# Optimization experiments

Measured on AMD Instinct MI355X. Metric: run time of the kernel, lower is better.

The kernel has to match this reference:

```python
import jax, jax.numpy as jnp
import numpy as np
from jax import lax

K = 3      # kernel size
PAD = 1    # padding (stride=1, dilation=1, single offset group)


def _deform_conv2d(x, off, weight, bias):
    # x: [B,C,H,W], off: [B,2*K*K,H,W] (y,x per tap), weight: [O,C,K,K], bias: [O]
    B, C, H, W = x.shape
    KK = K * K
    off = off.reshape(B, KK, 2, H, W)
    off_y, off_x = off[:, :, 0], off[:, :, 1]          # [B,KK,H,W]

    kh = jnp.repeat(jnp.arange(K, dtype=x.dtype), K)   # [KK] tap row offsets
    kw = jnp.tile(jnp.arange(K, dtype=x.dtype), K)     # [KK] tap col offsets
    py = (jnp.arange(H, dtype=x.dtype)[None, None, :, None] - PAD
          + kh[None, :, None, None] + off_y)           # [B,KK,H,W] sample rows
    px = (jnp.arange(W, dtype=x.dtype)[None, None, None, :] - PAD
          + kw[None, :, None, None] + off_x)           # [B,KK,H,W] sample cols

    y0 = jnp.floor(py); x0 = jnp.floor(px)
    wy1 = py - y0; wx1 = px - x0
    wy0 = 1.0 - wy1; wx0 = 1.0 - wx1

    bidx = jnp.arange(B)[:, None, None, None]

    def gather(iy, ix):
        # zero outside the input (torchvision semantics)
        valid = (iy >= 0) & (iy < H) & (ix >= 0) & (ix < W)
        iyc = jnp.clip(iy, 0, H - 1).astype(jnp.int32)
        ixc = jnp.clip(ix, 0, W - 1).astype(jnp.int32)
        v = x[bidx, :, iyc, ixc]                       # [B,KK,H,W,C]
        return v * valid[..., None].astype(x.dtype)

    samp = (gather(y0, x0)           * (wy0 * wx0)[..., None]
            + gather(y0, x0 + 1)     * (wy0 * wx1)[..., None]
            + gather(y0 + 1, x0)     * (wy1 * wx0)[..., None]
            + gather(y0 + 1, x0 + 1) * (wy1 * wx1)[..., None])  # [B,KK,H,W,C]

    w = weight.reshape(weight.shape[0], C, KK)          # [O,C,KK]
    out = jnp.einsum('bkhwc,ock->bohw', samp, w) + bias[None, :, None, None]
    return out


def setup_inputs() -> dict:
    key = jax.random.key(0)
    k1, k2, k3 = jax.random.split(key, 3)
    B, C, O, H, W = 4, 64, 64, 128, 128
    x = jax.random.normal(k1, (B, C, H, W), dtype=jnp.float32)
    offset_w = jax.random.normal(k2, (2 * K * K, C, 3, 3), dtype=jnp.float32) * 0.02
    offset_b = jnp.zeros((2 * K * K,), dtype=jnp.float32)
    weight = jax.random.normal(k3, (O, C, K, K), dtype=jnp.float32) * 0.01
    bias = jnp.zeros((O,), dtype=jnp.float32)
    return {"x": x, "offset_w": offset_w, "offset_b": offset_b,
            "weight": weight, "bias": bias}


def reference(x, offset_w, offset_b, weight, bias):
    # offset-predicting conv (3x3, pad 1)
    off = lax.conv_general_dilated(
        x, offset_w, window_strides=(1, 1), padding='SAME',
        dimension_numbers=('NCHW', 'OIHW', 'NCHW')) + offset_b[None, :, None, None]
    return _deform_conv2d(x, off, weight, bias)
```

## Files before the change

kernel.cpp:

```cpp
#include <hip/hip_runtime.h>
#include <hip/hip_bf16.h>


typedef short short8 __attribute__((ext_vector_type(8)));
typedef float f32x4 __attribute__((ext_vector_type(4)));

#define SROW 36
#define PROW 88

static __device__ inline short bf16s(float f) {
    __hip_bfloat16 h = __float2bfloat16(f);
    return *(short*)&h;
}
static __device__ inline float lo2f(unsigned u) { return __uint_as_float(u << 16); }
static __device__ inline float hi2f(unsigned u) { return __uint_as_float(u & 0xffff0000u); }

__global__ void prep_transpose_kernel(const float* __restrict__ x,
                                      __hip_bfloat16* __restrict__ xBp,
                                      const float* __restrict__ offset_w,
                                      const float* __restrict__ weight,
                                      __hip_bfloat16* __restrict__ Wb,
                                      __hip_bfloat16* __restrict__ OWb)
{
    __shared__ __align__(16) float lds[128 * 65];
    int raw = blockIdx.x;
    int t = threadIdx.x;

    if (raw >= 520) {
        int id = (raw - 520) * 256 + t;
        if (id < 36864) {
            int j    = id & 7;
            int lane = (id >> 3) & 63;
            int id3  = id >> 9;
            int s    = id3 % 18;
            int otile = id3 / 18;
            int n = lane & 15, q = lane >> 4;
            int kap = s * 32 + q * 8 + j;
            int k = kap >> 6, c = kap & 63;
            int o = otile * 16 + n;
            Wb[id] = __float2bfloat16(weight[(o * 64 + c) * 9 + k]);
        }
        int id2 = id - 36864;
        if (id2 >= 0 && id2 < 18432) {
            int j    = id2 & 7;
            int lane = (id2 >> 3) & 63;
            int id3  = id2 >> 9;
            int s    = id3 % 18;
            int ntile = id3 / 18;
            int n = lane & 15, q = lane >> 4;
            int kap = s * 32 + q * 8 + j;
            int k = kap >> 6, c = kap & 63;
            int o = ntile * 16 + n;
            float v = (o < 18) ? offset_w[(o * 64 + c) * 9 + k] : 0.0f;
            OWb[id2] = __float2bfloat16(v);
        }
        return;
    }

    int blk = (raw & 7) * 65 + (raw >> 3);
    int b = blk / 130, r = blk - b * 130;
    unsigned* rowp = (unsigned*)(xBp + (size_t)(b * 130 + r) * 130 * 64);
    if (r == 0 || r == 129) {
        uint4 z = {0u, 0u, 0u, 0u};
        for (int i = 0; i < 5; ++i) {
            int e = i * 256 + t;
            if (e < 1040) ((uint4*)rowp)[e] = z;
        }
        return;
    }
    int h = r - 1;
    const float4* x4 = (const float4*)x;
    size_t base4 = (size_t)b * 262144 + (size_t)h * 32;
#pragma unroll
    for (int i = 0; i < 8; ++i) {
        int idx = i * 256 + t;
        int c = idx >> 5, w4 = idx & 31;
        float4 v = x4[base4 + (size_t)c * 4096 + w4];
        int wb = w4 * 4;
        lds[(wb + 0) * 65 + c] = v.x;
        lds[(wb + 1) * 65 + c] = v.y;
        lds[(wb + 2) * 65 + c] = v.z;
        lds[(wb + 3) * 65 + c] = v.w;
    }
    __syncthreads();
    unsigned* dst = rowp + 32;
    for (int i = 0; i < 16; ++i) {
        int L = i * 256 + t;
        int ww = L >> 5, c2 = L & 31;
        float f0 = lds[ww * 65 + c2 * 2];
        float f1 = lds[ww * 65 + c2 * 2 + 1];
        unsigned pk = ((unsigned)bf16s(f0) & 0xffffu) | ((unsigned)bf16s(f1) << 16);
        dst[L] = pk;
    }
    if (t < 64) {
        int col = (t >> 5) * 129;
        rowp[col * 32 + (t & 31)] = 0u;
    }
}

template<int K0, int K1>
static __device__ inline void sample_taps(const __hip_bfloat16* __restrict__ xb8,
                                          const float* __restrict__ offL,
                                          short* __restrict__ sampB,
                                          int h, int w0, int p, int c8)
{
    constexpr int NT = K1 - K0;
    float wa[NT], wb_[NT], wc[NT], wd[NT];
    uint4 r0[NT], r1[NT], r2[NT], r3[NT];
#pragma unroll
    for (int i = 0; i < NT; ++i) {
        int k = K0 + i;
        float offy = offL[(2 * k) * 16 + p];
        float offx = offL[(2 * k + 1) * 16 + p];
        float py = (float)(h - 1 + (k / 3)) + offy;
        float px = (float)(w0 + p - 1 + (k % 3)) + offx;
        float y0f = floorf(py), x0f = floorf(px);
        float wy1 = py - y0f, wx1 = px - x0f;
        float wy0 = 1.0f - wy1, wx0 = 1.0f - wx1;
        int iy = (int)y0f, ix = (int)x0f;
        int iy0 = min(max(iy, -1), 128);
        int ix0 = min(max(ix, -1), 128);
        int iy1 = min(max(iy + 1, -1), 128);
        int ix1 = min(max(ix + 1, -1), 128);
        int rb0 = iy0 * 130, rb1 = iy1 * 130;
        r0[i] = *(const uint4*)(xb8 + (rb0 + ix0) * 64);
        r1[i] = *(const uint4*)(xb8 + (rb0 + ix1) * 64);
        r2[i] = *(const uint4*)(xb8 + (rb1 + ix0) * 64);
        r3[i] = *(const uint4*)(xb8 + (rb1 + ix1) * 64);
        wa[i] = wy0 * wx0;
        wb_[i] = wy0 * wx1;
        wc[i] = wy1 * wx0;
        wd[i] = wy1 * wx1;
    }
#pragma unroll
    for (int i = 0; i < NT; ++i) {
        int k = K0 + i;
        short8 pk;
#define SAMP1(idx, comp, EXT) { \
            float sv = fmaf(wd[i], EXT(r3[i].comp), fmaf(wc[i], EXT(r2[i].comp), \
                       fmaf(wb_[i], EXT(r1[i].comp), wa[i] * EXT(r0[i].comp)))); \
            pk[idx] = bf16s(sv); }
        SAMP1(0, x, lo2f) SAMP1(1, x, hi2f)
        SAMP1(2, y, lo2f) SAMP1(3, y, hi2f)
        SAMP1(4, z, lo2f) SAMP1(5, z, hi2f)
        SAMP1(6, w, lo2f) SAMP1(7, w, hi2f)
#undef SAMP1
        int s = 2 * k + (c8 >> 2);
        *(short8*)&sampB[(s * 16 + p) * SROW + (c8 & 3) * 8] = pk;
    }
}

__global__ __launch_bounds__(256, 3) void deform_kernel(
    const __hip_bfloat16* __restrict__ xBp,
    const __hip_bfloat16* __restrict__ Wb,
    const __hip_bfloat16* __restrict__ OWb,
    const float* __restrict__ offset_b,
    const float* __restrict__ bias,
    float* __restrict__ out)
{
    __shared__ __align__(16) short sampB[18 * 16 * SROW];
    __shared__ __align__(16) float offL[288];

    int t = threadIdx.x, wv = t >> 6, lane = t & 63;
    int bid = (blockIdx.x & 7) * 512 + (blockIdx.x >> 3);
    int b  = bid >> 10;
    int h  = (bid >> 3) & 127;
    int w0 = (bid & 7) << 4;

    short* patch = sampB;

    {
#pragma unroll
        for (int i = 0; i < 2; ++i) {
            int e = i * 256 + t;
            if (e < 432) {
                int px = e >> 3, part = e & 7;
                int row = px / 18, col = px - row * 18;
                const uint4* src = (const uint4*)(xBp +
                    ((size_t)((b * 130 + h + row) * 130) + w0 + col) * 64 + part * 8);
                *(uint4*)&patch[px * PROW + part * 8] = *src;
            }
        }
    }
    __syncthreads();

    if (wv < 2) {
        int n = lane & 15, q = lane >> 4;
        const short8* Bw = (const short8*)OWb + (wv * 18) * 64 + lane;
        f32x4 acc = {0.f, 0.f, 0.f, 0.f};
#pragma unroll
        for (int s = 0; s < 18; ++s) {
            int k = s >> 1;
            int ky = k / 3, kx = k - ky * 3;
            int pix = ky * 18 + n + kx;
            const short8 a = *(const short8*)&patch[pix * PROW + (s & 1) * 32 + q * 8];
            acc = __builtin_amdgcn_mfma_f32_16x16x32_bf16(a, Bw[s * 64], acc, 0, 0, 0);
        }
        int o = wv * 16 + n;
        if (o < 18) {
            float bo = offset_b[o];
#pragma unroll
            for (int r = 0; r < 4; ++r)
                offL[o * 16 + q * 4 + r] = acc[r] + bo;
        }
    }
    __syncthreads();

    {
        int g8 = lane >> 3, c8 = lane & 7;
        int p = (wv & 1) * 8 + g8;
        const __hip_bfloat16* xb8 = xBp + (size_t)b * (130 * 130 * 64) + c8 * 8 + 131 * 64;
        if (wv < 2) sample_taps<0, 4>(xb8, offL, sampB, h, w0, p, c8);
        else        sample_taps<4, 9>(xb8, offL, sampB, h, w0, p, c8);
    }
    __syncthreads();

    {
        int n = lane & 15, q = lane >> 4;
        int arow = n * SROW + q * 8;
        const short8* BwW = (const short8*)Wb + (wv * 18) * 64 + lane;
        f32x4 acc = {0.f, 0.f, 0.f, 0.f};
#pragma unroll
        for (int s = 0; s < 18; ++s) {
            const short8 a = *(const short8*)&sampB[s * (16 * SROW) + arow];
            acc = __builtin_amdgcn_mfma_f32_16x16x32_bf16(a, BwW[s * 64], acc, 0, 0, 0);
        }
        int o = wv * 16 + n;
        float bo = bias[o];
        float4 st = {acc[0] + bo, acc[1] + bo, acc[2] + bo, acc[3] + bo};
        *(float4*)&out[(((size_t)b * 64 + o) * 128 + h) * 128 + w0 + q * 4] = st;
    }
}

extern "C" void kernel_launch(void* const* d_in, const int* in_sizes, int n_in,
                              void* d_out, int out_size, void* d_ws, size_t ws_size,
                              hipStream_t stream) {
    const float* x        = (const float*)d_in[0];
    const float* offset_w = (const float*)d_in[1];
    const float* offset_b = (const float*)d_in[2];
    const float* weight   = (const float*)d_in[3];
    const float* bias     = (const float*)d_in[4];
    char* ws = (char*)d_ws;
    __hip_bfloat16* xBp = (__hip_bfloat16*)ws;
    __hip_bfloat16* Wb  = (__hip_bfloat16*)(ws + 8652800);
    __hip_bfloat16* OWb = (__hip_bfloat16*)(ws + 8652800 + 73728);
    float* outp = (float*)d_out;

    hipLaunchKernelGGL(prep_transpose_kernel, dim3(736),  dim3(256), 0, stream,
                       x, xBp, offset_w, weight, Wb, OWb);
    hipLaunchKernelGGL(deform_kernel,         dim3(4096), dim3(256), 0, stream,
                       xBp, Wb, OWb, offset_b, bias, outp);
}
```

Measured before the change: 106.0 us.

## Widen deform block tile to 32 pixels and reuse weights across two MFMAs

Each block now handles 32 output pixels of a row instead of 16, which halves the grid. The input halo patch (34 columns instead of 18) is shared by more outputs, and all four waves now join the offset-conv MFMAs. In the output GEMM each loaded weight fragment feeds two MFMAs, one per 16-pixel half. In exchange, LDS use per block roughly doubles, every thread samples all nine taps, and there are fewer blocks to spread across CUs.

```diff
diff --git a/kernel.cpp b/kernel.cpp
--- a/kernel.cpp
+++ b/kernel.cpp
@@ -110,8 +110,8 @@
 #pragma unroll
     for (int i = 0; i < NT; ++i) {
         int k = K0 + i;
-        float offy = offL[(2 * k) * 16 + p];
-        float offx = offL[(2 * k + 1) * 16 + p];
+        float offy = offL[(2 * k) * 32 + p];
+        float offx = offL[(2 * k + 1) * 32 + p];
         float py = (float)(h - 1 + (k / 3)) + offy;
         float px = (float)(w0 + p - 1 + (k % 3)) + offx;
         float y0f = floorf(py), x0f = floorf(px);
@@ -146,7 +146,7 @@
         SAMP1(6, w, lo2f) SAMP1(7, w, hi2f)
 #undef SAMP1
         int s = 2 * k + (c8 >> 2);
-        *(short8*)&sampB[(s * 16 + p) * SROW + (c8 & 3) * 8] = pk;
+        *(short8*)&sampB[(s * 32 + p) * SROW + (c8 & 3) * 8] = pk;
     }
 }
 
@@ -158,24 +158,24 @@
     const float* __restrict__ bias,
     float* __restrict__ out)
 {
-    __shared__ __align__(16) short sampB[18 * 16 * SROW];
-    __shared__ __align__(16) float offL[288];
+    __shared__ __align__(16) short sampB[18 * 32 * SROW];
+    __shared__ __align__(16) float offL[18 * 2 * 32 / 2 * 2];
 
     int t = threadIdx.x, wv = t >> 6, lane = t & 63;
-    int bid = (blockIdx.x & 7) * 512 + (blockIdx.x >> 3);
-    int b  = bid >> 10;
-    int h  = (bid >> 3) & 127;
-    int w0 = (bid & 7) << 4;
+    int bid = (blockIdx.x & 7) * 256 + (blockIdx.x >> 3);
+    int b  = bid >> 9;
+    int h  = (bid >> 2) & 127;
+    int w0 = (bid & 3) << 5;
 
     short* patch = sampB;
 
     {
 #pragma unroll
-        for (int i = 0; i < 2; ++i) {
+        for (int i = 0; i < 4; ++i) {
             int e = i * 256 + t;
-            if (e < 432) {
+            if (e < 816) {
                 int px = e >> 3, part = e & 7;
-                int row = px / 18, col = px - row * 18;
+                int row = px / 34, col = px - row * 34;
                 const uint4* src = (const uint4*)(xBp +
                     ((size_t)((b * 130 + h + row) * 130) + w0 + col) * 64 + part * 8);
                 *(uint4*)&patch[px * PROW + part * 8] = *src;
@@ -184,51 +184,58 @@
     }
     __syncthreads();
 
-    if (wv < 2) {
+    {
+        int ot = wv & 1, pt = wv >> 1;
         int n = lane & 15, q = lane >> 4;
-        const short8* Bw = (const short8*)OWb + (wv * 18) * 64 + lane;
+        const short8* Bw = (const short8*)OWb + (ot * 18) * 64 + lane;
         f32x4 acc = {0.f, 0.f, 0.f, 0.f};
 #pragma unroll
         for (int s = 0; s < 18; ++s) {
             int k = s >> 1;
             int ky = k / 3, kx = k - ky * 3;
-            int pix = ky * 18 + n + kx;
+            int pix = ky * 34 + pt * 16 + n + kx;
             const short8 a = *(const short8*)&patch[pix * PROW + (s & 1) * 32 + q * 8];
             acc = __builtin_amdgcn_mfma_f32_16x16x32_bf16(a, Bw[s * 64], acc, 0, 0, 0);
         }
-        int o = wv * 16 + n;
+        int o = ot * 16 + n;
         if (o < 18) {
             float bo = offset_b[o];
 #pragma unroll
             for (int r = 0; r < 4; ++r)
-                offL[o * 16 + q * 4 + r] = acc[r] + bo;
+                offL[o * 32 + pt * 16 + q * 4 + r] = acc[r] + bo;
         }
     }
     __syncthreads();
 
     {
         int g8 = lane >> 3, c8 = lane & 7;
-        int p = (wv & 1) * 8 + g8;
+        int p = wv * 8 + g8;
         const __hip_bfloat16* xb8 = xBp + (size_t)b * (130 * 130 * 64) + c8 * 8 + 131 * 64;
-        if (wv < 2) sample_taps<0, 4>(xb8, offL, sampB, h, w0, p, c8);
-        else        sample_taps<4, 9>(xb8, offL, sampB, h, w0, p, c8);
+        sample_taps<0, 4>(xb8, offL, sampB, h, w0, p, c8);
+        sample_taps<4, 9>(xb8, offL, sampB, h, w0, p, c8);
     }
     __syncthreads();
 
     {
         int n = lane & 15, q = lane >> 4;
-        int arow = n * SROW + q * 8;
         const short8* BwW = (const short8*)Wb + (wv * 18) * 64 + lane;
-        f32x4 acc = {0.f, 0.f, 0.f, 0.f};
+        f32x4 acc0 = {0.f, 0.f, 0.f, 0.f};
+        f32x4 acc1 = {0.f, 0.f, 0.f, 0.f};
 #pragma unroll
         for (int s = 0; s < 18; ++s) {
-            const short8 a = *(const short8*)&sampB[s * (16 * SROW) + arow];
-            acc = __builtin_amdgcn_mfma_f32_16x16x32_bf16(a, BwW[s * 64], acc, 0, 0, 0);
+            const short8 bw = BwW[s * 64];
+            const short8 a0 = *(const short8*)&sampB[(s * 32 + n) * SROW + q * 8];
+            const short8 a1 = *(const short8*)&sampB[(s * 32 + 16 + n) * SROW + q * 8];
+            acc0 = __builtin_amdgcn_mfma_f32_16x16x32_bf16(a0, bw, acc0, 0, 0, 0);
+            acc1 = __builtin_amdgcn_mfma_f32_16x16x32_bf16(a1, bw, acc1, 0, 0, 0);
         }
         int o = wv * 16 + n;
         float bo = bias[o];
-        float4 st = {acc[0] + bo, acc[1] + bo, acc[2] + bo, acc[3] + bo};
-        *(float4*)&out[(((size_t)b * 64 + o) * 128 + h) * 128 + w0 + q * 4] = st;
+        float* ob = &out[(((size_t)b * 64 + o) * 128 + h) * 128 + w0 + q * 4];
+        float4 st0 = {acc0[0] + bo, acc0[1] + bo, acc0[2] + bo, acc0[3] + bo};
+        float4 st1 = {acc1[0] + bo, acc1[1] + bo, acc1[2] + bo, acc1[3] + bo};
+        *(float4*)ob = st0;
+        *(float4*)(ob + 16) = st1;
     }
 }
 
@@ -248,6 +255,6 @@
 
     hipLaunchKernelGGL(prep_transpose_kernel, dim3(736),  dim3(256), 0, stream,
                        x, xBp, offset_w, weight, Wb, OWb);
-    hipLaunchKernelGGL(deform_kernel,         dim3(4096), dim3(256), 0, stream,
+    hipLaunchKernelGGL(deform_kernel,         dim3(2048), dim3(256), 0, stream,
                        xBp, Wb, OWb, offset_b, bias, outp);
 }
```

After: 103.9 us, median of 2. Within noise of the previous version (-1.9%).
